# Performance work log

Measured on AMD Instinct MI355X. Metric: run time of the kernel, lower is better.

## Reference

```python
import jax, jax.numpy as jnp
import numpy as np
from jax import lax

CONF_THR = 0.5
NMS_THR = 0.5
B, N, C = 2, 8192, 80


def setup_inputs() -> dict:
    key = jax.random.key(0)
    k1, k2, k3, k4 = jax.random.split(key, 4)
    cls_logits = jax.random.normal(k1, (B, N, C), dtype=jnp.float32)
    deltas = jax.random.normal(k2, (B, N, 4), dtype=jnp.float32) * 0.1
    # anchors: valid x1,y1,x2,y2 boxes in [0,1]
    ctr = jax.random.uniform(k3, (N, 2), minval=0.05, maxval=0.95)
    wh = jax.random.uniform(k4, (N, 2), minval=0.02, maxval=0.2)
    anchors = jnp.concatenate([ctr - 0.5 * wh, ctr + 0.5 * wh], axis=-1).astype(jnp.float32)
    return {"cls_logits": cls_logits, "deltas": deltas, "anchors": anchors}


def apply_deltas_to_anchors(deltas, anchors):
    aw = anchors[:, 2] - anchors[:, 0]
    ah = anchors[:, 3] - anchors[:, 1]
    acx = anchors[:, 0] + 0.5 * aw
    acy = anchors[:, 1] + 0.5 * ah
    dx, dy = deltas[..., 0], deltas[..., 1]
    dw = jnp.minimum(deltas[..., 2], 4.0)
    dh = jnp.minimum(deltas[..., 3], 4.0)
    pcx = dx * aw + acx
    pcy = dy * ah + acy
    pw = jnp.exp(dw) * aw
    ph = jnp.exp(dh) * ah
    boxes = jnp.stack([pcx - 0.5 * pw, pcy - 0.5 * ph,
                       pcx + 0.5 * pw, pcy + 0.5 * ph], axis=-1)
    return jnp.clip(boxes, 0.0, 1.0)


def iou_matrix(b):  # b: [N,4] -> [N,N]
    x1, y1, x2, y2 = b[:, 0], b[:, 1], b[:, 2], b[:, 3]
    area = (x2 - x1) * (y2 - y1)
    ix1 = jnp.maximum(x1[:, None], x1[None, :])
    iy1 = jnp.maximum(y1[:, None], y1[None, :])
    ix2 = jnp.minimum(x2[:, None], x2[None, :])
    iy2 = jnp.minimum(y2[:, None], y2[None, :])
    inter = jnp.clip(ix2 - ix1, 0.0) * jnp.clip(iy2 - iy1, 0.0)
    union = area[:, None] + area[None, :] - inter
    return inter / jnp.maximum(union, 1e-9)


def nms_keep(boxes, scores, valid, thr):
    """Greedy NMS; returns bool keep mask in original order (padded shape N)."""
    n = boxes.shape[0]
    order = jnp.argsort(-scores)
    bs = boxes[order]
    vs = valid[order]
    iou = iou_matrix(bs)  # [N,N] in score order
    idx = jnp.arange(n)

    def body(keep, i):
        suppressed = jnp.any((iou[i] > thr) & keep & (idx < i))
        k = vs[i] & ~suppressed
        keep = keep.at[i].set(k)
        return keep, None

    keep_sorted, _ = lax.scan(body, jnp.zeros(n, dtype=bool), idx)
    return jnp.zeros(n, dtype=bool).at[order].set(keep_sorted)


def reference(cls_logits, deltas, anchors):
    all_scores = jax.nn.sigmoid(cls_logits)                 # [B,N,C]
    boxes = apply_deltas_to_anchors(deltas, anchors)        # [B,N,4]
    max_scores = jnp.max(all_scores, axis=-1)               # [B,N]
    labels = jnp.argmax(all_scores, axis=-1)                # [B,N]
    conf_mask = max_scores > CONF_THR
    w = boxes[..., 2] - boxes[..., 0]
    h = boxes[..., 3] - boxes[..., 1]
    size_mask = (w > 0.01) & (h > 0.01) & (w < 0.99) & (h < 0.99)
    valid = conf_mask & size_mask
    keep = jax.vmap(nms_keep, in_axes=(0, 0, 0, None))(boxes, max_scores, valid, NMS_THR)
    # Padded (jit-friendly) equivalent of the ragged per-image outputs:
    return boxes, max_scores, labels, keep, all_scores
```

## Files before the change

kernel.cpp:

```cpp
#include <hip/hip_runtime.h>

constexpr int NB = 2;
constexpr int NN = 8192;
constexpr int NC = 80;
constexpr int ROWS = NN + 1;

constexpr size_t OFF_BOXES  = 0;
constexpr size_t OFF_SCORES = (size_t)NB * NN * 4;
constexpr size_t OFF_LABELS = OFF_SCORES + (size_t)NB * NN;
constexpr size_t OFF_KEEP   = OFF_LABELS + (size_t)NB * NN;
constexpr size_t OFF_ALL    = OFF_KEEP + (size_t)NB * NN;

constexpr size_t WS_KEYS  = 0;
constexpr size_t WS_VBYTE = WS_KEYS + (size_t)NB * NN * 8;
constexpr size_t WS_ORDER = WS_VBYTE + (size_t)NB * NN;
constexpr size_t WS_SBOX  = WS_ORDER + (size_t)NB * NN * 4;
constexpr size_t WS_VBITS = WS_SBOX + (size_t)NB * NN * 16;
constexpr size_t WS_MASK  = WS_VBITS + (size_t)NB * 128 * 8;
constexpr size_t WS_DNM   = WS_MASK + (size_t)NB * ROWS * 128 * 8;
constexpr size_t WS_PART  = WS_DNM + (size_t)NB * 128 * 4 * 64 * 8;
constexpr size_t WS_TOTAL = WS_PART + (size_t)NB * 8 * NN * 4;
constexpr size_t WS_TOTAL_OLD = WS_PART;
constexpr int DNM_WORDS = NB * 128 * 4 * 64;
constexpr int NSEG = 8;

typedef unsigned long long u64;

__device__ inline void lbar() {
  __builtin_amdgcn_s_waitcnt(0xc07f);
  __builtin_amdgcn_s_barrier();
}

__device__ inline u64 readlane64(u64 v, int src) {
  unsigned int lo = (unsigned int)__builtin_amdgcn_readlane((int)(unsigned int)v, src);
  unsigned int hi = (unsigned int)__builtin_amdgcn_readlane((int)(unsigned int)(v >> 32), src);
  return ((u64)hi << 32) | lo;
}

__device__ inline u64 readfirstlane64(u64 v) {
  unsigned int lo = (unsigned int)__builtin_amdgcn_readfirstlane((int)(unsigned int)v);
  unsigned int hi = (unsigned int)__builtin_amdgcn_readfirstlane((int)(unsigned int)(v >> 32));
  return ((u64)hi << 32) | lo;
}

__device__ inline float iou_pair(const float4 p, const float4 q) {
#pragma clang fp contract(off)
  float areaA = (p.z - p.x) * (p.w - p.y);
  float areaB = (q.z - q.x) * (q.w - q.y);
  float ix1 = fmaxf(p.x, q.x);
  float iy1 = fmaxf(p.y, q.y);
  float ix2 = fminf(p.z, q.z);
  float iy2 = fminf(p.w, q.w);
  float inter = fmaxf(ix2 - ix1, 0.0f) * fmaxf(iy2 - iy1, 0.0f);
  float uni = areaA + areaB - inter;
  return inter / fmaxf(uni, 1e-9f);
}

__device__ inline float clip01(float v) { return fminf(fmaxf(v, 0.0f), 1.0f); }

__global__ __launch_bounds__(256) void decode_kernel(
    const float* __restrict__ logits, const float4* __restrict__ deltas,
    const float4* __restrict__ anchors, float4* __restrict__ boxes_out,
    float* __restrict__ scores_out, float* __restrict__ labels_out,
    float* __restrict__ all_out, u64* __restrict__ keys,
    unsigned char* __restrict__ vbyte, u64* __restrict__ vbits) {
#pragma clang fp contract(off)
  if (blockIdx.x == 0 && threadIdx.x < NB * 128) vbits[threadIdx.x] = 0ull;
  int wid = (blockIdx.x * 256 + threadIdx.x) >> 6;
  int lane = threadIdx.x & 63;
  int n = wid & (NN - 1);
  size_t base = (size_t)wid * NC;

  float x0 = logits[base + lane];
  float sig0 = 1.0f / (1.0f + expf(-x0));
  all_out[base + lane] = sig0;
  float bs = sig0;
  int bidx = lane;
  if (lane < NC - 64) {
    float x1 = logits[base + 64 + lane];
    float sig1 = 1.0f / (1.0f + expf(-x1));
    all_out[base + 64 + lane] = sig1;
    if (sig1 > bs) { bs = sig1; bidx = lane + 64; }
  }
  for (int off = 32; off; off >>= 1) {
    float os = __shfl_xor(bs, off, 64);
    int oi = __shfl_xor(bidx, off, 64);
    if (os > bs || (os == bs && oi < bidx)) { bs = os; bidx = oi; }
  }
  if (lane == 0) {
    float4 d = deltas[wid];
    float4 a = anchors[n];
    float aw = a.z - a.x, ah = a.w - a.y;
    float acx = a.x + 0.5f * aw, acy = a.y + 0.5f * ah;
    float dw = fminf(d.z, 4.0f), dh = fminf(d.w, 4.0f);
    float pcx = d.x * aw + acx;
    float pcy = d.y * ah + acy;
    float pw = expf(dw) * aw;
    float ph = expf(dh) * ah;
    float4 bx;
    bx.x = clip01(pcx - 0.5f * pw);
    bx.y = clip01(pcy - 0.5f * ph);
    bx.z = clip01(pcx + 0.5f * pw);
    bx.w = clip01(pcy + 0.5f * ph);
    boxes_out[wid] = bx;
    scores_out[wid] = bs;
    labels_out[wid] = (float)bidx;
    float bw = bx.z - bx.x, bh = bx.w - bx.y;
    bool valid = (bs > 0.5f) && (bw > 0.01f) && (bh > 0.01f) &&
                 (bw < 0.99f) && (bh < 0.99f);
    vbyte[wid] = valid ? 1 : 0;
    keys[wid] = ((u64)__float_as_uint(bs) << 32) | (unsigned int)(NN - 1 - n);
  }
}

__global__ __launch_bounds__(1024) void rank_part_kernel(
    const u64* __restrict__ keys, int* __restrict__ part,
    u64* __restrict__ dnm) {
  int b = blockIdx.z, seg = blockIdx.y, rb = blockIdx.x;
  int gid = ((blockIdx.z * NSEG + blockIdx.y) * gridDim.x + blockIdx.x) * 1024 +
            threadIdx.x;
  if (gid < DNM_WORDS) dnm[gid] = 0ull;
  int r = threadIdx.x & 255;
  int q = threadIdx.x >> 8;
  int i = rb * 256 + r;
  const u64* kb = keys + (size_t)b * NN;
  u64 myk = kb[i];
  int cnt = 0;
  int j0 = seg * (NN / NSEG) + q * (NN / NSEG / 4);
  int j1 = j0 + NN / NSEG / 4;
#pragma unroll 8
  for (int j = j0; j < j1; ++j) {
    u64 kj = kb[j];
    cnt += (kj > myk) ? 1 : 0;
  }
  __shared__ unsigned short partl[4][256];
  partl[q][r] = (unsigned short)cnt;
  __syncthreads();
  if (threadIdx.x < 256) {
    int s = partl[0][r] + partl[1][r] + partl[2][r] + partl[3][r];
    part[((size_t)b * NSEG + seg) * NN + i] = s;
  }
}

__global__ __launch_bounds__(256) void rank_final_kernel(
    const int* __restrict__ part, const float4* __restrict__ boxes,
    const unsigned char* __restrict__ vbyte, int* __restrict__ order,
    float4* __restrict__ sbox, u64* __restrict__ vbits) {
  int b = blockIdx.y;
  int i = blockIdx.x * 256 + threadIdx.x;
  const int* pb = part + (size_t)b * NSEG * NN + i;
  int rank = 0;
#pragma unroll
  for (int s = 0; s < NSEG; ++s) rank += pb[(size_t)s * NN];
  order[(size_t)b * NN + rank] = i;
  sbox[(size_t)b * NN + rank] = boxes[(size_t)b * NN + i];
  if (vbyte[(size_t)b * NN + i])
    atomicOr(&vbits[b * 128 + (rank >> 6)], 1ull << (rank & 63));
}

__global__ __launch_bounds__(1024) void rank_kernel(
    const u64* __restrict__ keys, const float4* __restrict__ boxes,
    const unsigned char* __restrict__ vbyte, int* __restrict__ order,
    float4* __restrict__ sbox, u64* __restrict__ vbits,
    u64* __restrict__ dnm) {
  int b = blockIdx.y;
  int gid = (blockIdx.y * gridDim.x + blockIdx.x) * 1024 + threadIdx.x;
  for (int z = gid; z < DNM_WORDS; z += 65536) dnm[z] = 0ull;
  int r = threadIdx.x & 255;
  int q = threadIdx.x >> 8;
  int i = blockIdx.x * 256 + r;
  const u64* kb = keys + (size_t)b * NN;
  u64 myk = kb[i];
  int cnt = 0;
  int j0 = q * (NN / 4), j1 = j0 + NN / 4;
#pragma unroll 8
  for (int j = j0; j < j1; ++j) {
    u64 kj = kb[j];
    cnt += (kj > myk) ? 1 : 0;
  }
  __shared__ unsigned short part[4][256];
  part[q][r] = (unsigned short)cnt;
  __syncthreads();
  if (threadIdx.x < 256) {
    int rank = part[0][r] + part[1][r] + part[2][r] + part[3][r];
    order[(size_t)b * NN + rank] = i;
    sbox[(size_t)b * NN + rank] = boxes[(size_t)b * NN + i];
    if (vbyte[(size_t)b * NN + i])
      atomicOr(&vbits[b * 128 + (rank >> 6)], 1ull << (rank & 63));
  }
}

__global__ __launch_bounds__(64) void build_kernel(
    const float4* __restrict__ sbox, u64* __restrict__ mask,
    u64* __restrict__ dnm) {
  int byq = blockIdx.y, bxq = blockIdx.x, b = blockIdx.z;
  int by, bx;
  if (bxq >= byq) {
    by = byq; bx = bxq;
  } else if (byq == 64) {
    return;
  } else {
    by = 128 - byq; bx = 127 - bxq;
  }
  int lane = threadIdx.x;
  __shared__ float4 cb[64];
  cb[lane] = sbox[(size_t)b * NN + bx * 64 + lane];
  __syncthreads();
  int i = by * 64 + lane;
  float4 rb = sbox[(size_t)b * NN + i];
  u64 word = 0;
  if (bx == by) {
    for (int jj = 0; jj < 64; ++jj)
      if (iou_pair(rb, cb[jj]) > 0.5f) word |= 1ull << jj;
    word &= ~(1ull << lane);
    u64 lmask = (1ull << lane) - 1ull;
    mask[((size_t)b * ROWS + i) * 128 + bx] = word & ~lmask;
    dnm[(((size_t)b * 128 + by) * 4 + 0) * 64 + lane] = word & lmask;
  } else {
    for (int jj = 0; jj < 64; ++jj)
      if (iou_pair(rb, cb[jj]) > 0.5f) word |= 1ull << jj;
    mask[((size_t)b * ROWS + i) * 128 + bx] = word;
    int dq = bx - by;
    if (dq < 4) dnm[(((size_t)b * 128 + by) * 4 + dq) * 64 + lane] = word;
  }
}

struct TSet {
  ulonglong2 t0, t1, t2, t3, t4, t5, t6, t7, t8, t9;
};

__global__ __launch_bounds__(512) void reduce_kernel(
    u64* __restrict__ mask, const u64* __restrict__ vbits,
    const u64* __restrict__ dnm, const int* __restrict__ order,
    float* __restrict__ keep_out) {
  int b = blockIdx.x, tid = threadIdx.x;
  int lane = tid & 63, wave = tid >> 6;
  __shared__ u64 s_remv[128];
  __shared__ u64 s_keep[128];
  __shared__ int s_rowlist[2][80];
  u64* mbz = mask + (size_t)b * ROWS * 128;
  const u64* mb = mbz;
  const u64* dn = dnm + (size_t)b * 128 * 4 * 64;

  for (int w = tid; w < 128; w += 512) {
    s_remv[w] = 0ull;
    mbz[(size_t)NN * 128 + w] = 0ull;
  }
  if (tid < 160) s_rowlist[tid / 80][tid % 80] = NN;

  u64 va = 0, vb2 = 0;
  u64 dA = 0, nA = 0, mA = 0, oA = 0, dB = 0, nB = 0, mB = 0, oB = 0;
  u64 dC = 0, nC = 0, mC = 0, oC = 0, dD = 0, nD = 0, mD = 0, oD = 0;
  if (wave == 0) {
    va = vbits[b * 128 + 2 * lane];
    vb2 = vbits[b * 128 + 2 * lane + 1];
    const u64* r0 = dn + lane;
    dA = r0[0]; nA = r0[64]; mA = r0[128]; oA = r0[192];
    const u64* r1 = dn + 4 * 64 + lane;
    dB = r1[0]; nB = r1[64]; mB = r1[128]; oB = r1[192];
  }
  TSet U{}, V{};
  int w0i = 2 * lane;
  __syncthreads();

  auto serial_body = [&](int c, u64 dcur, u64 ncur, u64 mcur, u64 ocur,
                         u64& dnew, u64& nnew, u64& mnew, u64& onew) {
    {
      int cp = (c + 2 < 128) ? (c + 2) : 127;
      const u64* rp = dn + (size_t)cp * 4 * 64 + lane;
      dnew = rp[0]; nnew = rp[64]; mnew = rp[128]; onew = rp[192];
    }
    int par = c & 1;
    u64 rm = s_remv[c];
    u64 vbw = readlane64(par ? vb2 : va, c >> 1);
    u64 cand = readfirstlane64(vbw & ~rm);
    u64 kept = cand;
    while (true) {
      u64 sup = __ballot((dcur & kept) != 0ull);
      u64 nk = cand & ~sup;
      if (nk == kept) break;
      kept = nk;
    }
    bool isk = (kept >> lane) & 1;
    if (c + 1 < 128 && isk && ncur) atomicOr(&s_remv[c + 1], ncur);
    if (c + 2 < 128 && isk && mcur) atomicOr(&s_remv[c + 2], mcur);
    if (c + 3 < 128 && isk && ocur) atomicOr(&s_remv[c + 3], ocur);
    s_rowlist[par][lane] = NN;
    if (isk) {
      int pos = __popcll(kept & ((1ull << lane) - 1ull));
      s_rowlist[par][pos] = c * 64 + lane;
    }
    if (lane == 0) s_keep[c] = kept;
  };

  auto bg_body = [&](int c, TSet& T) {
    u64 ax = T.t0.x | T.t1.x | T.t2.x | T.t3.x | T.t4.x | T.t5.x | T.t6.x |
             T.t7.x | T.t8.x | T.t9.x;
    u64 ay = T.t0.y | T.t1.y | T.t2.y | T.t3.y | T.t4.y | T.t5.y | T.t6.y |
             T.t7.y | T.t8.y | T.t9.y;
    int sc = (c + 1) & ~1;
    int wx = sc + w0i, wy = wx + 1;
    if (wx > c && wx < 128 && ax) atomicOr(&s_remv[wx], ax);
    if (wy > c && wy < 128 && ay) atomicOr(&s_remv[wy], ay);
    const int* rl = s_rowlist[(c - 1) & 1];
    int base = wave - 1;
    int si = (c + 3) & ~1;
    int w = si + w0i;
    if (w > 126) w = 126;
    const u64* mw = mb + w;
    T.t0 = *(const ulonglong2*)(mw + (size_t)rl[base] * 128);
    T.t1 = *(const ulonglong2*)(mw + (size_t)rl[base + 7] * 128);
    T.t2 = *(const ulonglong2*)(mw + (size_t)rl[base + 14] * 128);
    T.t3 = *(const ulonglong2*)(mw + (size_t)rl[base + 21] * 128);
    T.t4 = *(const ulonglong2*)(mw + (size_t)rl[base + 28] * 128);
    T.t5 = *(const ulonglong2*)(mw + (size_t)rl[base + 35] * 128);
    T.t6 = *(const ulonglong2*)(mw + (size_t)rl[base + 42] * 128);
    T.t7 = *(const ulonglong2*)(mw + (size_t)rl[base + 49] * 128);
    T.t8 = *(const ulonglong2*)(mw + (size_t)rl[base + 56] * 128);
    T.t9 = *(const ulonglong2*)(mw + (size_t)rl[base + 63] * 128);
  };

  for (int c = 0; c < 128; c += 4) {
    if (wave == 0) serial_body(c, dA, nA, mA, oA, dC, nC, mC, oC);
    else bg_body(c, U);
    lbar();
    if (wave == 0) serial_body(c + 1, dB, nB, mB, oB, dD, nD, mD, oD);
    else bg_body(c + 1, V);
    lbar();
    if (wave == 0) serial_body(c + 2, dC, nC, mC, oC, dA, nA, mA, oA);
    else bg_body(c + 2, U);
    lbar();
    if (wave == 0) serial_body(c + 3, dD, nD, mD, oD, dB, nB, mB, oB);
    else bg_body(c + 3, V);
    lbar();
  }

  for (int p = tid; p < NN; p += 512) {
    int orig = order[(size_t)b * NN + p];
    keep_out[(size_t)b * NN + orig] =
        ((s_keep[p >> 6] >> (p & 63)) & 1) ? 1.0f : 0.0f;
  }
}

__global__ __launch_bounds__(1024) void nms_fallback(
    const float4* __restrict__ sbox, const u64* __restrict__ vbits,
    const int* __restrict__ order, float* __restrict__ keep_out) {
  int b = blockIdx.x, tid = threadIdx.x;
  __shared__ u64 dead[128];
  __shared__ int s_next;
  __shared__ float4 s_box;
  for (int w = tid; w < 128; w += 1024) dead[w] = ~vbits[b * 128 + w];
  for (int p = tid; p < NN; p += 1024)
    keep_out[(size_t)b * NN + order[(size_t)b * NN + p]] = 0.0f;
  __syncthreads();
  int i = 0;
  while (true) {
    if (tid == 0) {
      int nxt = NN;
      int w = i >> 6;
      u64 live = ~dead[w] & (~0ull << (i & 63));
      while (true) {
        if (live) { nxt = w * 64 + __builtin_ctzll(live); break; }
        if (++w >= 128) break;
        live = ~dead[w];
      }
      s_next = nxt;
      if (nxt < NN) {
        s_box = sbox[(size_t)b * NN + nxt];
        keep_out[(size_t)b * NN + order[(size_t)b * NN + nxt]] = 1.0f;
      }
    }
    __syncthreads();
    i = s_next;
    if (i >= NN) break;
    float4 kb = s_box;
    for (int j = i + 1 + tid; j < NN; j += 1024) {
      if (iou_pair(kb, sbox[(size_t)b * NN + j]) > 0.5f)
        atomicOr(&dead[j >> 6], 1ull << (j & 63));
    }
    __syncthreads();
    i = i + 1;
  }
}

extern "C" void kernel_launch(void* const* d_in, const int* in_sizes, int n_in,
                              void* d_out, int out_size, void* d_ws, size_t ws_size,
                              hipStream_t stream) {
  const float* logits = (const float*)d_in[0];
  const float4* deltas = (const float4*)d_in[1];
  const float4* anchors = (const float4*)d_in[2];
  float* out = (float*)d_out;
  float4* boxes_out = (float4*)(out + OFF_BOXES);
  float* scores_out = out + OFF_SCORES;
  float* labels_out = out + OFF_LABELS;
  float* keep_out = out + OFF_KEEP;
  float* all_out = out + OFF_ALL;

  char* ws = (char*)d_ws;
  u64* keys = (u64*)(ws + WS_KEYS);
  unsigned char* vbyte = (unsigned char*)(ws + WS_VBYTE);
  int* order = (int*)(ws + WS_ORDER);
  float4* sbox = (float4*)(ws + WS_SBOX);
  u64* vbits = (u64*)(ws + WS_VBITS);
  u64* mask = (u64*)(ws + WS_MASK);
  u64* dnm = (u64*)(ws + WS_DNM);
  int* part = (int*)(ws + WS_PART);

  decode_kernel<<<dim3(NB * NN / 4), dim3(256), 0, stream>>>(
      logits, deltas, anchors, boxes_out, scores_out, labels_out, all_out,
      keys, vbyte, vbits);
  if (ws_size >= WS_TOTAL) {
    rank_part_kernel<<<dim3(NN / 256, NSEG, NB), dim3(1024), 0, stream>>>(
        keys, part, dnm);
    rank_final_kernel<<<dim3(NN / 256, NB), dim3(256), 0, stream>>>(
        part, (const float4*)boxes_out, vbyte, order, sbox, vbits);
    build_kernel<<<dim3(128, 65, NB), dim3(64), 0, stream>>>(sbox, mask, dnm);
    reduce_kernel<<<dim3(NB), dim3(512), 0, stream>>>(mask, vbits, dnm, order,
                                                      keep_out);
  } else if (ws_size >= WS_TOTAL_OLD) {
    rank_kernel<<<dim3(NN / 256, NB), dim3(1024), 0, stream>>>(
        keys, (const float4*)boxes_out, vbyte, order, sbox, vbits, dnm);
    build_kernel<<<dim3(128, 65, NB), dim3(64), 0, stream>>>(sbox, mask, dnm);
    reduce_kernel<<<dim3(NB), dim3(512), 0, stream>>>(mask, vbits, dnm, order,
                                                      keep_out);
  } else {
    rank_kernel<<<dim3(NN / 256, NB), dim3(1024), 0, stream>>>(
        keys, (const float4*)boxes_out, vbyte, order, sbox, vbits, dnm);
    nms_fallback<<<dim3(NB), dim3(1024), 0, stream>>>(sbox, vbits, order,
                                                      keep_out);
  }
}
```

Baseline: 248.0 us.

## Add sparse adjacency-list NMS reduction with dense fallback on overflow

The build kernel now also records, for each sorted box, a compact list of up to 64 later overlapping box indices via atomic degree counters. A new single-wave reduce_sparse kernel walks the blocks serially and sets suppression bits from these short lists, so it no longer scans the dense bitmask with background waves. If any row overflows the cap, the dense reducer runs instead. The final keep scatter moves into a separate parallel kernel. This adds more workspace, extra atomics in build, and two more kernel launches.

```diff
diff --git a/kernel.cpp b/kernel.cpp
--- a/kernel.cpp
+++ b/kernel.cpp
@@ -21,10 +21,16 @@
 constexpr size_t WS_PART  = WS_DNM + (size_t)NB * 128 * 4 * 64 * 8;
 constexpr size_t WS_TOTAL = WS_PART + (size_t)NB * 8 * NN * 4;
 constexpr size_t WS_TOTAL_OLD = WS_PART;
+constexpr int ROW_CAP = 64;
+constexpr size_t WS_RDEG = WS_TOTAL;
+constexpr size_t WS_RENT = WS_RDEG + (size_t)NB * NN * 4;
+constexpr size_t WS_OVF  = WS_RENT + (size_t)NB * NN * ROW_CAP * 2;
+constexpr size_t WS_TOTAL_SPARSE = WS_OVF + 64;
 constexpr int DNM_WORDS = NB * 128 * 4 * 64;
 constexpr int NSEG = 8;
 
 typedef unsigned long long u64;
+typedef __attribute__((ext_vector_type(2))) unsigned long long u64x2;
 
 __device__ inline void lbar() {
   __builtin_amdgcn_s_waitcnt(0xc07f);
@@ -115,26 +121,30 @@
 
 __global__ __launch_bounds__(1024) void rank_part_kernel(
     const u64* __restrict__ keys, int* __restrict__ part,
-    u64* __restrict__ dnm) {
+    u64* __restrict__ dnm, unsigned int* rowdeg, unsigned int* ovf) {
   int b = blockIdx.z, seg = blockIdx.y, rb = blockIdx.x;
   int gid = ((blockIdx.z * NSEG + blockIdx.y) * gridDim.x + blockIdx.x) * 1024 +
             threadIdx.x;
   if (gid < DNM_WORDS) dnm[gid] = 0ull;
+  if (rowdeg) {
+    if (gid < NB * NN) rowdeg[gid] = 0u;
+    if (gid < NB) ovf[gid] = 0u;
+  }
   int r = threadIdx.x & 255;
   int q = threadIdx.x >> 8;
   int i = rb * 256 + r;
   const u64* kb = keys + (size_t)b * NN;
   u64 myk = kb[i];
-  int cnt = 0;
+  int cnt2 = 0;
   int j0 = seg * (NN / NSEG) + q * (NN / NSEG / 4);
   int j1 = j0 + NN / NSEG / 4;
 #pragma unroll 8
   for (int j = j0; j < j1; ++j) {
     u64 kj = kb[j];
-    cnt += (kj > myk) ? 1 : 0;
+    cnt2 += (kj > myk) ? 1 : 0;
   }
   __shared__ unsigned short partl[4][256];
-  partl[q][r] = (unsigned short)cnt;
+  partl[q][r] = (unsigned short)cnt2;
   __syncthreads();
   if (threadIdx.x < 256) {
     int s = partl[0][r] + partl[1][r] + partl[2][r] + partl[3][r];
@@ -192,7 +202,8 @@
 
 __global__ __launch_bounds__(64) void build_kernel(
     const float4* __restrict__ sbox, u64* __restrict__ mask,
-    u64* __restrict__ dnm) {
+    u64* __restrict__ dnm, unsigned int* rowdeg,
+    unsigned short* rowent, unsigned int* ovf) {
   int byq = blockIdx.y, bxq = blockIdx.x, b = blockIdx.z;
   int by, bx;
   if (bxq >= byq) {
@@ -209,31 +220,131 @@
   int i = by * 64 + lane;
   float4 rb = sbox[(size_t)b * NN + i];
   u64 word = 0;
+  for (int jj = 0; jj < 64; ++jj)
+    if (iou_pair(rb, cb[jj]) > 0.5f) word |= 1ull << jj;
+  u64 ent;
   if (bx == by) {
-    for (int jj = 0; jj < 64; ++jj)
-      if (iou_pair(rb, cb[jj]) > 0.5f) word |= 1ull << jj;
     word &= ~(1ull << lane);
     u64 lmask = (1ull << lane) - 1ull;
     mask[((size_t)b * ROWS + i) * 128 + bx] = word & ~lmask;
     dnm[(((size_t)b * 128 + by) * 4 + 0) * 64 + lane] = word & lmask;
+    ent = word & ~lmask;
   } else {
-    for (int jj = 0; jj < 64; ++jj)
-      if (iou_pair(rb, cb[jj]) > 0.5f) word |= 1ull << jj;
     mask[((size_t)b * ROWS + i) * 128 + bx] = word;
     int dq = bx - by;
     if (dq < 4) dnm[(((size_t)b * 128 + by) * 4 + dq) * 64 + lane] = word;
-  }
+    ent = word;
+  }
+  if (rowdeg && ent) {
+    int wcnt = __popcll(ent);
+    unsigned base = atomicAdd(&rowdeg[(size_t)b * NN + i], (unsigned)wcnt);
+    if (base + (unsigned)wcnt <= (unsigned)ROW_CAP) {
+      unsigned short* dst = rowent + ((size_t)b * NN + i) * ROW_CAP + base;
+      int k = 0;
+      u64 t = ent;
+      while (t) {
+        int bit = __builtin_ctzll(t);
+        dst[k++] = (unsigned short)(bx * 64 + bit);
+        t &= t - 1;
+      }
+    } else {
+      atomicOr(&ovf[b], 1u);
+    }
+  }
+}
+
+__global__ __launch_bounds__(64) void reduce_sparse(
+    const u64* __restrict__ vbits, const u64* __restrict__ dnm,
+    const unsigned int* __restrict__ rowdeg,
+    const unsigned short* __restrict__ rowent,
+    const unsigned int* __restrict__ ovf, u64* __restrict__ keepw) {
+  int b = blockIdx.x, lane = threadIdx.x;
+  if (ovf[b]) return;
+  __shared__ u64 s_remv[128];
+  __shared__ u64 s_keep[128];
+  s_remv[2 * lane] = 0ull;
+  s_remv[2 * lane + 1] = 0ull;
+  u64 va = vbits[b * 128 + 2 * lane];
+  u64 vb2 = vbits[b * 128 + 2 * lane + 1];
+  const u64* dnb = dnm + (size_t)b * 128 * 4 * 64;
+  const unsigned int* dgb = rowdeg + (size_t)b * NN;
+  const unsigned short* reb = rowent + (size_t)b * NN * ROW_CAP;
+
+  u64 dA = dnb[lane];
+  unsigned gA = dgb[lane];
+  const u64x2* pA = (const u64x2*)(reb + (size_t)lane * ROW_CAP);
+  u64x2 eA0 = pA[0], eA1 = pA[1], eA2 = pA[2], eA3 = pA[3];
+  u64 dB = dnb[4 * 64 + lane];
+  unsigned gB = dgb[64 + lane];
+  const u64x2* pB = (const u64x2*)(reb + (size_t)(64 + lane) * ROW_CAP);
+  u64x2 eB0 = pB[0], eB1 = pB[1], eB2 = pB[2], eB3 = pB[3];
+  u64 dC = 0, dD = 0;
+  unsigned gC = 0, gD = 0;
+  u64x2 eC0{}, eC1{}, eC2{}, eC3{}, eD0{}, eD1{}, eD2{}, eD3{};
+
+  auto body = [&](int c, u64 dcur, unsigned gcur, u64x2 e0, u64x2 e1,
+                  u64x2 e2, u64x2 e3, u64& dnw, unsigned& gnw, u64x2& n0,
+                  u64x2& n1, u64x2& n2, u64x2& n3) {
+    int cp = (c + 2 < 128) ? c + 2 : 127;
+    dnw = dnb[(size_t)cp * 4 * 64 + lane];
+    gnw = dgb[cp * 64 + lane];
+    const u64x2* np = (const u64x2*)(reb + (size_t)(cp * 64 + lane) * ROW_CAP);
+    n0 = np[0]; n1 = np[1]; n2 = np[2]; n3 = np[3];
+    u64 rm = s_remv[c];
+    u64 vbw = readlane64((c & 1) ? vb2 : va, c >> 1);
+    u64 cand = readfirstlane64(vbw & ~rm);
+    u64 kept = cand;
+    while (true) {
+      u64 sup = __ballot((dcur & kept) != 0ull);
+      u64 nk = cand & ~sup;
+      if (nk == kept) break;
+      kept = nk;
+    }
+    bool isk = (kept >> lane) & 1;
+    int deg = (int)gcur;
+    if (isk && deg > 0) {
+      int lim = deg < 32 ? deg : 32;
+#pragma unroll
+      for (int k = 0; k < 32; ++k) {
+        if (k < lim) {
+          u64 src = (k < 16)
+                        ? ((k < 8) ? ((k < 4) ? e0[0] : e0[1])
+                                   : ((k < 12) ? e1[0] : e1[1]))
+                        : ((k < 24) ? ((k < 20) ? e2[0] : e2[1])
+                                    : ((k < 28) ? e3[0] : e3[1]));
+          int j = (int)((src >> ((k & 3) * 16)) & 0xFFFFull);
+          atomicOr(&s_remv[j >> 6], 1ull << (j & 63));
+        }
+      }
+      for (int k = 32; k < deg; ++k) {
+        int j = reb[(size_t)(c * 64 + lane) * ROW_CAP + k];
+        atomicOr(&s_remv[j >> 6], 1ull << (j & 63));
+      }
+    }
+    if (lane == 0) s_keep[c] = kept;
+  };
+
+  for (int c = 0; c < 128; c += 4) {
+    body(c + 0, dA, gA, eA0, eA1, eA2, eA3, dC, gC, eC0, eC1, eC2, eC3);
+    body(c + 1, dB, gB, eB0, eB1, eB2, eB3, dD, gD, eD0, eD1, eD2, eD3);
+    body(c + 2, dC, gC, eC0, eC1, eC2, eC3, dA, gA, eA0, eA1, eA2, eA3);
+    body(c + 3, dD, gD, eD0, eD1, eD2, eD3, dB, gB, eB0, eB1, eB2, eB3);
+  }
+
+  keepw[b * 128 + 2 * lane] = s_keep[2 * lane];
+  keepw[b * 128 + 2 * lane + 1] = s_keep[2 * lane + 1];
 }
 
 struct TSet {
-  ulonglong2 t0, t1, t2, t3, t4, t5, t6, t7, t8, t9;
+  u64x2 t0, t1, t2, t3, t4, t5, t6, t7, t8, t9;
 };
 
-__global__ __launch_bounds__(512) void reduce_kernel(
+__global__ __launch_bounds__(512) void reduce_dense(
     u64* __restrict__ mask, const u64* __restrict__ vbits,
-    const u64* __restrict__ dnm, const int* __restrict__ order,
-    float* __restrict__ keep_out) {
+    const u64* __restrict__ dnm, const unsigned int* __restrict__ ovf,
+    u64* __restrict__ keepw) {
   int b = blockIdx.x, tid = threadIdx.x;
+  if (ovf && ovf[b] == 0) return;
   int lane = tid & 63, wave = tid >> 6;
   __shared__ u64 s_remv[128];
   __shared__ u64 s_keep[128];
@@ -265,11 +376,9 @@
 
   auto serial_body = [&](int c, u64 dcur, u64 ncur, u64 mcur, u64 ocur,
                          u64& dnew, u64& nnew, u64& mnew, u64& onew) {
-    {
-      int cp = (c + 2 < 128) ? (c + 2) : 127;
-      const u64* rp = dn + (size_t)cp * 4 * 64 + lane;
-      dnew = rp[0]; nnew = rp[64]; mnew = rp[128]; onew = rp[192];
-    }
+    int cp = (c + 2 < 128) ? (c + 2) : 127;
+    const u64* rp = dn + (size_t)cp * 4 * 64 + lane;
+    dnew = rp[0]; nnew = rp[64]; mnew = rp[128]; onew = rp[192];
     int par = c & 1;
     u64 rm = s_remv[c];
     u64 vbw = readlane64(par ? vb2 : va, c >> 1);
@@ -294,10 +403,10 @@
   };
 
   auto bg_body = [&](int c, TSet& T) {
-    u64 ax = T.t0.x | T.t1.x | T.t2.x | T.t3.x | T.t4.x | T.t5.x | T.t6.x |
-             T.t7.x | T.t8.x | T.t9.x;
-    u64 ay = T.t0.y | T.t1.y | T.t2.y | T.t3.y | T.t4.y | T.t5.y | T.t6.y |
-             T.t7.y | T.t8.y | T.t9.y;
+    u64 ax = T.t0[0] | T.t1[0] | T.t2[0] | T.t3[0] | T.t4[0] | T.t5[0] |
+             T.t6[0] | T.t7[0] | T.t8[0] | T.t9[0];
+    u64 ay = T.t0[1] | T.t1[1] | T.t2[1] | T.t3[1] | T.t4[1] | T.t5[1] |
+             T.t6[1] | T.t7[1] | T.t8[1] | T.t9[1];
     int sc = (c + 1) & ~1;
     int wx = sc + w0i, wy = wx + 1;
     if (wx > c && wx < 128 && ax) atomicOr(&s_remv[wx], ax);
@@ -306,18 +415,23 @@
     int base = wave - 1;
     int si = (c + 3) & ~1;
     int w = si + w0i;
-    if (w > 126) w = 126;
+    bool wok = w < 128;
     const u64* mw = mb + w;
-    T.t0 = *(const ulonglong2*)(mw + (size_t)rl[base] * 128);
-    T.t1 = *(const ulonglong2*)(mw + (size_t)rl[base + 7] * 128);
-    T.t2 = *(const ulonglong2*)(mw + (size_t)rl[base + 14] * 128);
-    T.t3 = *(const ulonglong2*)(mw + (size_t)rl[base + 21] * 128);
-    T.t4 = *(const ulonglong2*)(mw + (size_t)rl[base + 28] * 128);
-    T.t5 = *(const ulonglong2*)(mw + (size_t)rl[base + 35] * 128);
-    T.t6 = *(const ulonglong2*)(mw + (size_t)rl[base + 42] * 128);
-    T.t7 = *(const ulonglong2*)(mw + (size_t)rl[base + 49] * 128);
-    T.t8 = *(const ulonglong2*)(mw + (size_t)rl[base + 56] * 128);
-    T.t9 = *(const ulonglong2*)(mw + (size_t)rl[base + 63] * 128);
+    const u64* zp = mbz + (size_t)NN * 128;
+    int r0 = rl[base], r1 = rl[base + 7], r2 = rl[base + 14],
+        r3 = rl[base + 21], r4 = rl[base + 28], r5 = rl[base + 35],
+        r6 = rl[base + 42], r7 = rl[base + 49], r8 = rl[base + 56],
+        r9 = rl[base + 63];
+    T.t0 = *(const u64x2*)((wok && r0 != NN) ? mw + (size_t)r0 * 128 : zp);
+    T.t1 = *(const u64x2*)((wok && r1 != NN) ? mw + (size_t)r1 * 128 : zp);
+    T.t2 = *(const u64x2*)((wok && r2 != NN) ? mw + (size_t)r2 * 128 : zp);
+    T.t3 = *(const u64x2*)((wok && r3 != NN) ? mw + (size_t)r3 * 128 : zp);
+    T.t4 = *(const u64x2*)((wok && r4 != NN) ? mw + (size_t)r4 * 128 : zp);
+    T.t5 = *(const u64x2*)((wok && r5 != NN) ? mw + (size_t)r5 * 128 : zp);
+    T.t6 = *(const u64x2*)((wok && r6 != NN) ? mw + (size_t)r6 * 128 : zp);
+    T.t7 = *(const u64x2*)((wok && r7 != NN) ? mw + (size_t)r7 * 128 : zp);
+    T.t8 = *(const u64x2*)((wok && r8 != NN) ? mw + (size_t)r8 * 128 : zp);
+    T.t9 = *(const u64x2*)((wok && r9 != NN) ? mw + (size_t)r9 * 128 : zp);
   };
 
   for (int c = 0; c < 128; c += 4) {
@@ -335,11 +449,18 @@
     lbar();
   }
 
-  for (int p = tid; p < NN; p += 512) {
-    int orig = order[(size_t)b * NN + p];
-    keep_out[(size_t)b * NN + orig] =
-        ((s_keep[p >> 6] >> (p & 63)) & 1) ? 1.0f : 0.0f;
-  }
+  __syncthreads();
+  for (int w = tid; w < 128; w += 512) keepw[b * 128 + w] = s_keep[w];
+}
+
+__global__ __launch_bounds__(256) void scatter_keep(
+    const u64* __restrict__ keepw, const int* __restrict__ order,
+    float* __restrict__ keep_out) {
+  int b = blockIdx.y;
+  int p = blockIdx.x * 256 + threadIdx.x;
+  int orig = order[(size_t)b * NN + p];
+  keep_out[(size_t)b * NN + orig] =
+      ((keepw[b * 128 + (p >> 6)] >> (p & 63)) & 1) ? 1.0f : 0.0f;
 }
 
 __global__ __launch_bounds__(1024) void nms_fallback(
@@ -405,24 +526,47 @@
   u64* mask = (u64*)(ws + WS_MASK);
   u64* dnm = (u64*)(ws + WS_DNM);
   int* part = (int*)(ws + WS_PART);
+  unsigned int* rowdeg = (unsigned int*)(ws + WS_RDEG);
+  unsigned short* rowent = (unsigned short*)(ws + WS_RENT);
+  unsigned int* ovf = (unsigned int*)(ws + WS_OVF);
+  u64* keepw = (u64*)(ws + WS_KEYS);
 
   decode_kernel<<<dim3(NB * NN / 4), dim3(256), 0, stream>>>(
       logits, deltas, anchors, boxes_out, scores_out, labels_out, all_out,
       keys, vbyte, vbits);
-  if (ws_size >= WS_TOTAL) {
+  if (ws_size >= WS_TOTAL_SPARSE) {
     rank_part_kernel<<<dim3(NN / 256, NSEG, NB), dim3(1024), 0, stream>>>(
-        keys, part, dnm);
+        keys, part, dnm, rowdeg, ovf);
     rank_final_kernel<<<dim3(NN / 256, NB), dim3(256), 0, stream>>>(
         part, (const float4*)boxes_out, vbyte, order, sbox, vbits);
-    build_kernel<<<dim3(128, 65, NB), dim3(64), 0, stream>>>(sbox, mask, dnm);
-    reduce_kernel<<<dim3(NB), dim3(512), 0, stream>>>(mask, vbits, dnm, order,
-                                                      keep_out);
+    build_kernel<<<dim3(128, 65, NB), dim3(64), 0, stream>>>(
+        sbox, mask, dnm, rowdeg, rowent, ovf);
+    reduce_sparse<<<dim3(NB), dim3(64), 0, stream>>>(vbits, dnm, rowdeg,
+                                                     rowent, ovf, keepw);
+    reduce_dense<<<dim3(NB), dim3(512), 0, stream>>>(mask, vbits, dnm, ovf,
+                                                     keepw);
+    scatter_keep<<<dim3(NN / 256, NB), dim3(256), 0, stream>>>(keepw, order,
+                                                               keep_out);
+  } else if (ws_size >= WS_TOTAL) {
+    rank_part_kernel<<<dim3(NN / 256, NSEG, NB), dim3(1024), 0, stream>>>(
+        keys, part, dnm, nullptr, nullptr);
+    rank_final_kernel<<<dim3(NN / 256, NB), dim3(256), 0, stream>>>(
+        part, (const float4*)boxes_out, vbyte, order, sbox, vbits);
+    build_kernel<<<dim3(128, 65, NB), dim3(64), 0, stream>>>(
+        sbox, mask, dnm, nullptr, nullptr, nullptr);
+    reduce_dense<<<dim3(NB), dim3(512), 0, stream>>>(mask, vbits, dnm, nullptr,
+                                                     keepw);
+    scatter_keep<<<dim3(NN / 256, NB), dim3(256), 0, stream>>>(keepw, order,
+                                                               keep_out);
   } else if (ws_size >= WS_TOTAL_OLD) {
     rank_kernel<<<dim3(NN / 256, NB), dim3(1024), 0, stream>>>(
         keys, (const float4*)boxes_out, vbyte, order, sbox, vbits, dnm);
-    build_kernel<<<dim3(128, 65, NB), dim3(64), 0, stream>>>(sbox, mask, dnm);
-    reduce_kernel<<<dim3(NB), dim3(512), 0, stream>>>(mask, vbits, dnm, order,
-                                                      keep_out);
+    build_kernel<<<dim3(128, 65, NB), dim3(64), 0, stream>>>(
+        sbox, mask, dnm, nullptr, nullptr, nullptr);
+    reduce_dense<<<dim3(NB), dim3(512), 0, stream>>>(mask, vbits, dnm, nullptr,
+                                                     keepw);
+    scatter_keep<<<dim3(NN / 256, NB), dim3(256), 0, stream>>>(keepw, order,
+                                                               keep_out);
   } else {
     rank_kernel<<<dim3(NN / 256, NB), dim3(1024), 0, stream>>>(
         keys, (const float4*)boxes_out, vbyte, order, sbox, vbits, dnm);
```

New measurement: 274.8 us. 10.8% more time.

## Process 128-box chunks per serial NMS step and split keep scatter into own kernel

Applied to the files above, without the earlier changes.

Adds a reduce128 kernel whose serial wave resolves two 64-bit words (128 sorted boxes) per step. This halves the number of barrier-separated serial iterations, with a 1024-thread block doing background row merging. The build kernel writes a new per-row dnm2 layout holding the within-chunk transposed masks and the next two chunks. The final keep scatter moves out of the single-block reduce into a parallel scatter_keep kernel. The new path is chosen only when the workspace is large enough, and it adds an extra launch plus a more complex fixed-point loop per step.

```diff
diff --git a/kernel.cpp b/kernel.cpp
--- a/kernel.cpp
+++ b/kernel.cpp
@@ -21,10 +21,14 @@
 constexpr size_t WS_PART  = WS_DNM + (size_t)NB * 128 * 4 * 64 * 8;
 constexpr size_t WS_TOTAL = WS_PART + (size_t)NB * 8 * NN * 4;
 constexpr size_t WS_TOTAL_OLD = WS_PART;
+constexpr size_t WS_DNM2 = WS_TOTAL;
+constexpr size_t WS_TOTAL_128 = WS_DNM2 + (size_t)NB * NN * 6 * 8;
 constexpr int DNM_WORDS = NB * 128 * 4 * 64;
+constexpr int DNM2_WORDS = NB * NN * 6;
 constexpr int NSEG = 8;
 
 typedef unsigned long long u64;
+typedef __attribute__((ext_vector_type(2))) unsigned long long u64x2;
 
 __device__ inline void lbar() {
   __builtin_amdgcn_s_waitcnt(0xc07f);
@@ -115,26 +119,30 @@
 
 __global__ __launch_bounds__(1024) void rank_part_kernel(
     const u64* __restrict__ keys, int* __restrict__ part,
-    u64* __restrict__ dnm) {
+    u64* __restrict__ dnm, u64* __restrict__ dnm2) {
   int b = blockIdx.z, seg = blockIdx.y, rb = blockIdx.x;
   int gid = ((blockIdx.z * NSEG + blockIdx.y) * gridDim.x + blockIdx.x) * 1024 +
             threadIdx.x;
-  if (gid < DNM_WORDS) dnm[gid] = 0ull;
+  if (dnm2) {
+    if (gid < DNM2_WORDS) dnm2[gid] = 0ull;
+  } else {
+    if (gid < DNM_WORDS) dnm[gid] = 0ull;
+  }
   int r = threadIdx.x & 255;
   int q = threadIdx.x >> 8;
   int i = rb * 256 + r;
   const u64* kb = keys + (size_t)b * NN;
   u64 myk = kb[i];
-  int cnt = 0;
+  int cnt2 = 0;
   int j0 = seg * (NN / NSEG) + q * (NN / NSEG / 4);
   int j1 = j0 + NN / NSEG / 4;
 #pragma unroll 8
   for (int j = j0; j < j1; ++j) {
     u64 kj = kb[j];
-    cnt += (kj > myk) ? 1 : 0;
+    cnt2 += (kj > myk) ? 1 : 0;
   }
   __shared__ unsigned short partl[4][256];
-  partl[q][r] = (unsigned short)cnt;
+  partl[q][r] = (unsigned short)cnt2;
   __syncthreads();
   if (threadIdx.x < 256) {
     int s = partl[0][r] + partl[1][r] + partl[2][r] + partl[3][r];
@@ -192,7 +200,7 @@
 
 __global__ __launch_bounds__(64) void build_kernel(
     const float4* __restrict__ sbox, u64* __restrict__ mask,
-    u64* __restrict__ dnm) {
+    u64* __restrict__ dnm, u64* __restrict__ dnm2) {
   int byq = blockIdx.y, bxq = blockIdx.x, b = blockIdx.z;
   int by, bx;
   if (bxq >= byq) {
@@ -204,35 +212,199 @@
   }
   int lane = threadIdx.x;
   __shared__ float4 cb[64];
+  __shared__ float4 rbs[64];
   cb[lane] = sbox[(size_t)b * NN + bx * 64 + lane];
   __syncthreads();
   int i = by * 64 + lane;
   float4 rb = sbox[(size_t)b * NN + i];
   u64 word = 0;
+  for (int jj = 0; jj < 64; ++jj)
+    if (iou_pair(rb, cb[jj]) > 0.5f) word |= 1ull << jj;
   if (bx == by) {
-    for (int jj = 0; jj < 64; ++jj)
-      if (iou_pair(rb, cb[jj]) > 0.5f) word |= 1ull << jj;
     word &= ~(1ull << lane);
     u64 lmask = (1ull << lane) - 1ull;
     mask[((size_t)b * ROWS + i) * 128 + bx] = word & ~lmask;
-    dnm[(((size_t)b * 128 + by) * 4 + 0) * 64 + lane] = word & lmask;
+    if (dnm2) {
+      dnm2[((size_t)b * NN + i) * 6 + ((by & 1) ? 1 : 0)] = word & lmask;
+    } else {
+      dnm[(((size_t)b * 128 + by) * 4 + 0) * 64 + lane] = word & lmask;
+    }
   } else {
-    for (int jj = 0; jj < 64; ++jj)
-      if (iou_pair(rb, cb[jj]) > 0.5f) word |= 1ull << jj;
     mask[((size_t)b * ROWS + i) * 128 + bx] = word;
-    int dq = bx - by;
-    if (dq < 4) dnm[(((size_t)b * 128 + by) * 4 + dq) * 64 + lane] = word;
+    if (dnm2) {
+      int dq = (bx >> 1) - (by >> 1);
+      if (dq == 0) {
+        rbs[lane] = rb;
+        __syncthreads();
+        float4 myc = cb[lane];
+        u64 cm = 0;
+        for (int jj = 0; jj < 64; ++jj)
+          if (iou_pair(myc, rbs[jj]) > 0.5f) cm |= 1ull << jj;
+        dnm2[((size_t)b * NN + bx * 64 + lane) * 6 + 0] = cm;
+      } else if (dq == 1) {
+        dnm2[((size_t)b * NN + i) * 6 + 2 + (bx & 1)] = word;
+      } else if (dq == 2) {
+        dnm2[((size_t)b * NN + i) * 6 + 4 + (bx & 1)] = word;
+      }
+    } else {
+      int dq = bx - by;
+      if (dq < 4) dnm[(((size_t)b * 128 + by) * 4 + dq) * 64 + lane] = word;
+    }
+  }
+}
+
+__global__ __launch_bounds__(1024) void reduce128(
+    u64* __restrict__ mask, const u64* __restrict__ vbits,
+    const u64* __restrict__ dnm2, u64* __restrict__ keepw) {
+  int b = blockIdx.x, tid = threadIdx.x;
+  int lane = tid & 63, wave = tid >> 6;
+  __shared__ u64 s_remv[128];
+  __shared__ u64 s_keep[128];
+  __shared__ int s_rowlist[2][144];
+  u64* mbz = mask + (size_t)b * ROWS * 128;
+  const u64* mb = mbz;
+  const u64* d2 = dnm2 + (size_t)b * NN * 6;
+
+  for (int w = tid; w < 128; w += 1024) {
+    s_remv[w] = 0ull;
+    mbz[(size_t)NN * 128 + w] = 0ull;
+  }
+  for (int w = tid; w < 288; w += 1024) s_rowlist[w / 144][w % 144] = NN;
+
+  u64 va = 0, vb2 = 0;
+  u64 Adl0 = 0, Aln0 = 0, Aln1 = 0, Alm0 = 0, Alm1 = 0;
+  u64 Adh0 = 0, Adh1 = 0, Ahn0 = 0, Ahn1 = 0, Ahm0 = 0, Ahm1 = 0;
+  u64 Bdl0 = 0, Bln0 = 0, Bln1 = 0, Blm0 = 0, Blm1 = 0;
+  u64 Bdh0 = 0, Bdh1 = 0, Bhn0 = 0, Bhn1 = 0, Bhm0 = 0, Bhm1 = 0;
+  if (wave == 0) {
+    va = vbits[b * 128 + 2 * lane];
+    vb2 = vbits[b * 128 + 2 * lane + 1];
+    const u64* plo = d2 + (size_t)(0 * 128 + lane) * 6;
+    Adl0 = plo[0]; Aln0 = plo[2]; Aln1 = plo[3]; Alm0 = plo[4]; Alm1 = plo[5];
+    const u64* phi = d2 + (size_t)(0 * 128 + 64 + lane) * 6;
+    Adh0 = phi[0]; Adh1 = phi[1]; Ahn0 = phi[2]; Ahn1 = phi[3];
+    Ahm0 = phi[4]; Ahm1 = phi[5];
+    const u64* qlo = d2 + (size_t)(1 * 128 + lane) * 6;
+    Bdl0 = qlo[0]; Bln0 = qlo[2]; Bln1 = qlo[3]; Blm0 = qlo[4]; Blm1 = qlo[5];
+    const u64* qhi = d2 + (size_t)(1 * 128 + 64 + lane) * 6;
+    Bdh0 = qhi[0]; Bdh1 = qhi[1]; Bhn0 = qhi[2]; Bhn1 = qhi[3];
+    Bhm0 = qhi[4]; Bhm1 = qhi[5];
+  }
+  u64x2 t0{}, t1{}, t2{}, t3{}, t4{}, t5{}, t6{}, t7{}, t8{};
+  __syncthreads();
+
+  auto sbody = [&](int c, u64& dl0, u64& ln0, u64& ln1, u64& lm0, u64& lm1,
+                   u64& dh0, u64& dh1, u64& hn0, u64& hn1, u64& hm0,
+                   u64& hm1) {
+    u64 rm0 = s_remv[2 * c];
+    u64 rm1 = s_remv[2 * c + 1];
+    u64 cand0 = readfirstlane64(readlane64(va, c) & ~rm0);
+    u64 cand1 = readfirstlane64(readlane64(vb2, c) & ~rm1);
+    u64 K0 = cand0, K1 = cand1;
+    while (true) {
+      u64 s0 = __ballot((dl0 & K0) != 0ull);
+      u64 s1 = __ballot(((dh0 & K0) | (dh1 & K1)) != 0ull);
+      u64 n0 = cand0 & ~s0, n1 = cand1 & ~s1;
+      if (n0 == K0 && n1 == K1) break;
+      K0 = n0;
+      K1 = n1;
+    }
+    bool klo = (K0 >> lane) & 1, khi = (K1 >> lane) & 1;
+    int wd = 2 * c + 2;
+    if (klo) {
+      if (wd < 128 && ln0) atomicOr(&s_remv[wd], ln0);
+      if (wd + 1 < 128 && ln1) atomicOr(&s_remv[wd + 1], ln1);
+      if (wd + 2 < 128 && lm0) atomicOr(&s_remv[wd + 2], lm0);
+      if (wd + 3 < 128 && lm1) atomicOr(&s_remv[wd + 3], lm1);
+    }
+    if (khi) {
+      if (wd < 128 && hn0) atomicOr(&s_remv[wd], hn0);
+      if (wd + 1 < 128 && hn1) atomicOr(&s_remv[wd + 1], hn1);
+      if (wd + 2 < 128 && hm0) atomicOr(&s_remv[wd + 2], hm0);
+      if (wd + 3 < 128 && hm1) atomicOr(&s_remv[wd + 3], hm1);
+    }
+    int par = c & 1;
+    s_rowlist[par][lane] = NN;
+    s_rowlist[par][64 + lane] = NN;
+    if (lane < 16) s_rowlist[par][128 + lane] = NN;
+    if (klo) {
+      int pos = __popcll(K0 & ((1ull << lane) - 1ull));
+      s_rowlist[par][pos] = c * 128 + lane;
+    }
+    if (khi) {
+      int pos = __popcll(K0) + __popcll(K1 & ((1ull << lane) - 1ull));
+      s_rowlist[par][pos] = c * 128 + 64 + lane;
+    }
+    if (lane == 0) {
+      s_keep[2 * c] = K0;
+      s_keep[2 * c + 1] = K1;
+    }
+    int cp = (c + 2 < 64) ? c + 2 : 63;
+    const u64* plo = d2 + (size_t)(cp * 128 + lane) * 6;
+    dl0 = plo[0]; ln0 = plo[2]; ln1 = plo[3]; lm0 = plo[4]; lm1 = plo[5];
+    const u64* phi = d2 + (size_t)(cp * 128 + 64 + lane) * 6;
+    dh0 = phi[0]; dh1 = phi[1]; hn0 = phi[2]; hn1 = phi[3];
+    hm0 = phi[4]; hm1 = phi[5];
+  };
+
+  auto bgbody = [&](int c) {
+    u64 ax = t0[0] | t1[0] | t2[0] | t3[0] | t4[0] | t5[0] | t6[0] | t7[0] |
+             t8[0];
+    u64 ay = t0[1] | t1[1] | t2[1] | t3[1] | t4[1] | t5[1] | t6[1] | t7[1] |
+             t8[1];
+    int sp = 2 * c + 2;
+    int wx = sp + 2 * lane, wy = wx + 1;
+    if (wx < 128 && ax) atomicOr(&s_remv[wx], ax);
+    if (wy < 128 && ay) atomicOr(&s_remv[wy], ay);
+    const int* rl = s_rowlist[(c - 1) & 1];
+    int base = wave - 1;
+    int si = 2 * c + 4;
+    int w = si + 2 * lane;
+    bool wok = w < 128;
+    const u64* mw = mb + w;
+    const u64* zp = mbz + (size_t)NN * 128;
+    int r0 = rl[base], r1 = rl[base + 15], r2 = rl[base + 30],
+        r3 = rl[base + 45], r4 = rl[base + 60], r5 = rl[base + 75],
+        r6 = rl[base + 90], r7 = rl[base + 105], r8 = rl[base + 120];
+    t0 = *(const u64x2*)((wok && r0 != NN) ? mw + (size_t)r0 * 128 : zp);
+    t1 = *(const u64x2*)((wok && r1 != NN) ? mw + (size_t)r1 * 128 : zp);
+    t2 = *(const u64x2*)((wok && r2 != NN) ? mw + (size_t)r2 * 128 : zp);
+    t3 = *(const u64x2*)((wok && r3 != NN) ? mw + (size_t)r3 * 128 : zp);
+    t4 = *(const u64x2*)((wok && r4 != NN) ? mw + (size_t)r4 * 128 : zp);
+    t5 = *(const u64x2*)((wok && r5 != NN) ? mw + (size_t)r5 * 128 : zp);
+    t6 = *(const u64x2*)((wok && r6 != NN) ? mw + (size_t)r6 * 128 : zp);
+    t7 = *(const u64x2*)((wok && r7 != NN) ? mw + (size_t)r7 * 128 : zp);
+    t8 = *(const u64x2*)((wok && r8 != NN) ? mw + (size_t)r8 * 128 : zp);
+  };
+
+  for (int c = 0; c < 64; c += 2) {
+    if (wave == 0)
+      sbody(c, Adl0, Aln0, Aln1, Alm0, Alm1, Adh0, Adh1, Ahn0, Ahn1, Ahm0,
+            Ahm1);
+    else
+      bgbody(c);
+    lbar();
+    if (wave == 0)
+      sbody(c + 1, Bdl0, Bln0, Bln1, Blm0, Blm1, Bdh0, Bdh1, Bhn0, Bhn1, Bhm0,
+            Bhm1);
+    else
+      bgbody(c + 1);
+    lbar();
+  }
+
+  if (wave == 0) {
+    keepw[b * 128 + 2 * lane] = s_keep[2 * lane];
+    keepw[b * 128 + 2 * lane + 1] = s_keep[2 * lane + 1];
   }
 }
 
 struct TSet {
-  ulonglong2 t0, t1, t2, t3, t4, t5, t6, t7, t8, t9;
+  u64x2 t0, t1, t2, t3, t4, t5, t6, t7, t8, t9;
 };
 
-__global__ __launch_bounds__(512) void reduce_kernel(
+__global__ __launch_bounds__(512) void reduce_dense(
     u64* __restrict__ mask, const u64* __restrict__ vbits,
-    const u64* __restrict__ dnm, const int* __restrict__ order,
-    float* __restrict__ keep_out) {
+    const u64* __restrict__ dnm, u64* __restrict__ keepw) {
   int b = blockIdx.x, tid = threadIdx.x;
   int lane = tid & 63, wave = tid >> 6;
   __shared__ u64 s_remv[128];
@@ -265,11 +437,9 @@
 
   auto serial_body = [&](int c, u64 dcur, u64 ncur, u64 mcur, u64 ocur,
                          u64& dnew, u64& nnew, u64& mnew, u64& onew) {
-    {
-      int cp = (c + 2 < 128) ? (c + 2) : 127;
-      const u64* rp = dn + (size_t)cp * 4 * 64 + lane;
-      dnew = rp[0]; nnew = rp[64]; mnew = rp[128]; onew = rp[192];
-    }
+    int cp = (c + 2 < 128) ? (c + 2) : 127;
+    const u64* rp = dn + (size_t)cp * 4 * 64 + lane;
+    dnew = rp[0]; nnew = rp[64]; mnew = rp[128]; onew = rp[192];
     int par = c & 1;
     u64 rm = s_remv[c];
     u64 vbw = readlane64(par ? vb2 : va, c >> 1);
@@ -294,10 +464,10 @@
   };
 
   auto bg_body = [&](int c, TSet& T) {
-    u64 ax = T.t0.x | T.t1.x | T.t2.x | T.t3.x | T.t4.x | T.t5.x | T.t6.x |
-             T.t7.x | T.t8.x | T.t9.x;
-    u64 ay = T.t0.y | T.t1.y | T.t2.y | T.t3.y | T.t4.y | T.t5.y | T.t6.y |
-             T.t7.y | T.t8.y | T.t9.y;
+    u64 ax = T.t0[0] | T.t1[0] | T.t2[0] | T.t3[0] | T.t4[0] | T.t5[0] |
+             T.t6[0] | T.t7[0] | T.t8[0] | T.t9[0];
+    u64 ay = T.t0[1] | T.t1[1] | T.t2[1] | T.t3[1] | T.t4[1] | T.t5[1] |
+             T.t6[1] | T.t7[1] | T.t8[1] | T.t9[1];
     int sc = (c + 1) & ~1;
     int wx = sc + w0i, wy = wx + 1;
     if (wx > c && wx < 128 && ax) atomicOr(&s_remv[wx], ax);
@@ -306,18 +476,23 @@
     int base = wave - 1;
     int si = (c + 3) & ~1;
     int w = si + w0i;
-    if (w > 126) w = 126;
+    bool wok = w < 128;
     const u64* mw = mb + w;
-    T.t0 = *(const ulonglong2*)(mw + (size_t)rl[base] * 128);
-    T.t1 = *(const ulonglong2*)(mw + (size_t)rl[base + 7] * 128);
-    T.t2 = *(const ulonglong2*)(mw + (size_t)rl[base + 14] * 128);
-    T.t3 = *(const ulonglong2*)(mw + (size_t)rl[base + 21] * 128);
-    T.t4 = *(const ulonglong2*)(mw + (size_t)rl[base + 28] * 128);
-    T.t5 = *(const ulonglong2*)(mw + (size_t)rl[base + 35] * 128);
-    T.t6 = *(const ulonglong2*)(mw + (size_t)rl[base + 42] * 128);
-    T.t7 = *(const ulonglong2*)(mw + (size_t)rl[base + 49] * 128);
-    T.t8 = *(const ulonglong2*)(mw + (size_t)rl[base + 56] * 128);
-    T.t9 = *(const ulonglong2*)(mw + (size_t)rl[base + 63] * 128);
+    const u64* zp = mbz + (size_t)NN * 128;
+    int r0 = rl[base], r1 = rl[base + 7], r2 = rl[base + 14],
+        r3 = rl[base + 21], r4 = rl[base + 28], r5 = rl[base + 35],
+        r6 = rl[base + 42], r7 = rl[base + 49], r8 = rl[base + 56],
+        r9 = rl[base + 63];
+    T.t0 = *(const u64x2*)((wok && r0 != NN) ? mw + (size_t)r0 * 128 : zp);
+    T.t1 = *(const u64x2*)((wok && r1 != NN) ? mw + (size_t)r1 * 128 : zp);
+    T.t2 = *(const u64x2*)((wok && r2 != NN) ? mw + (size_t)r2 * 128 : zp);
+    T.t3 = *(const u64x2*)((wok && r3 != NN) ? mw + (size_t)r3 * 128 : zp);
+    T.t4 = *(const u64x2*)((wok && r4 != NN) ? mw + (size_t)r4 * 128 : zp);
+    T.t5 = *(const u64x2*)((wok && r5 != NN) ? mw + (size_t)r5 * 128 : zp);
+    T.t6 = *(const u64x2*)((wok && r6 != NN) ? mw + (size_t)r6 * 128 : zp);
+    T.t7 = *(const u64x2*)((wok && r7 != NN) ? mw + (size_t)r7 * 128 : zp);
+    T.t8 = *(const u64x2*)((wok && r8 != NN) ? mw + (size_t)r8 * 128 : zp);
+    T.t9 = *(const u64x2*)((wok && r9 != NN) ? mw + (size_t)r9 * 128 : zp);
   };
 
   for (int c = 0; c < 128; c += 4) {
@@ -335,11 +510,18 @@
     lbar();
   }
 
-  for (int p = tid; p < NN; p += 512) {
-    int orig = order[(size_t)b * NN + p];
-    keep_out[(size_t)b * NN + orig] =
-        ((s_keep[p >> 6] >> (p & 63)) & 1) ? 1.0f : 0.0f;
-  }
+  __syncthreads();
+  for (int w = tid; w < 128; w += 512) keepw[b * 128 + w] = s_keep[w];
+}
+
+__global__ __launch_bounds__(256) void scatter_keep(
+    const u64* __restrict__ keepw, const int* __restrict__ order,
+    float* __restrict__ keep_out) {
+  int b = blockIdx.y;
+  int p = blockIdx.x * 256 + threadIdx.x;
+  int orig = order[(size_t)b * NN + p];
+  keep_out[(size_t)b * NN + orig] =
+      ((keepw[b * 128 + (p >> 6)] >> (p & 63)) & 1) ? 1.0f : 0.0f;
 }
 
 __global__ __launch_bounds__(1024) void nms_fallback(
@@ -405,24 +587,40 @@
   u64* mask = (u64*)(ws + WS_MASK);
   u64* dnm = (u64*)(ws + WS_DNM);
   int* part = (int*)(ws + WS_PART);
+  u64* dnm2 = (u64*)(ws + WS_DNM2);
+  u64* keepw = (u64*)(ws + WS_KEYS);
 
   decode_kernel<<<dim3(NB * NN / 4), dim3(256), 0, stream>>>(
       logits, deltas, anchors, boxes_out, scores_out, labels_out, all_out,
       keys, vbyte, vbits);
-  if (ws_size >= WS_TOTAL) {
+  if (ws_size >= WS_TOTAL_128) {
     rank_part_kernel<<<dim3(NN / 256, NSEG, NB), dim3(1024), 0, stream>>>(
-        keys, part, dnm);
+        keys, part, dnm, dnm2);
     rank_final_kernel<<<dim3(NN / 256, NB), dim3(256), 0, stream>>>(
         part, (const float4*)boxes_out, vbyte, order, sbox, vbits);
-    build_kernel<<<dim3(128, 65, NB), dim3(64), 0, stream>>>(sbox, mask, dnm);
-    reduce_kernel<<<dim3(NB), dim3(512), 0, stream>>>(mask, vbits, dnm, order,
-                                                      keep_out);
+    build_kernel<<<dim3(128, 65, NB), dim3(64), 0, stream>>>(sbox, mask, dnm,
+                                                             dnm2);
+    reduce128<<<dim3(NB), dim3(1024), 0, stream>>>(mask, vbits, dnm2, keepw);
+    scatter_keep<<<dim3(NN / 256, NB), dim3(256), 0, stream>>>(keepw, order,
+                                                               keep_out);
+  } else if (ws_size >= WS_TOTAL) {
+    rank_part_kernel<<<dim3(NN / 256, NSEG, NB), dim3(1024), 0, stream>>>(
+        keys, part, dnm, nullptr);
+    rank_final_kernel<<<dim3(NN / 256, NB), dim3(256), 0, stream>>>(
+        part, (const float4*)boxes_out, vbyte, order, sbox, vbits);
+    build_kernel<<<dim3(128, 65, NB), dim3(64), 0, stream>>>(sbox, mask, dnm,
+                                                             nullptr);
+    reduce_dense<<<dim3(NB), dim3(512), 0, stream>>>(mask, vbits, dnm, keepw);
+    scatter_keep<<<dim3(NN / 256, NB), dim3(256), 0, stream>>>(keepw, order,
+                                                               keep_out);
   } else if (ws_size >= WS_TOTAL_OLD) {
     rank_kernel<<<dim3(NN / 256, NB), dim3(1024), 0, stream>>>(
         keys, (const float4*)boxes_out, vbyte, order, sbox, vbits, dnm);
-    build_kernel<<<dim3(128, 65, NB), dim3(64), 0, stream>>>(sbox, mask, dnm);
-    reduce_kernel<<<dim3(NB), dim3(512), 0, stream>>>(mask, vbits, dnm, order,
-                                                      keep_out);
+    build_kernel<<<dim3(128, 65, NB), dim3(64), 0, stream>>>(sbox, mask, dnm,
+                                                             nullptr);
+    reduce_dense<<<dim3(NB), dim3(512), 0, stream>>>(mask, vbits, dnm, keepw);
+    scatter_keep<<<dim3(NN / 256, NB), dim3(256), 0, stream>>>(keepw, order,
+                                                               keep_out);
   } else {
     rank_kernel<<<dim3(NN / 256, NB), dim3(1024), 0, stream>>>(
         keys, (const float4*)boxes_out, vbyte, order, sbox, vbits, dnm);
```

New measurement: 251.6 us. Within noise of the previous version (+1.4%).
